# Optimization experiments

Measured on AMD Instinct MI355X. Metric: run time of the kernel, lower is better.

## Reference

```python
import jax, jax.numpy as jnp
from jax import lax
import numpy as np

N_CENTER, N_NEAR, COUT = 1024, 32, 256


def fps(xyz, m):
    # farthest point sampling -> [B, m] int32 indices
    B, N, _ = xyz.shape
    dist0 = jnp.full((B, N), 1e10, xyz.dtype)
    far0 = jnp.zeros((B,), jnp.int32)

    def step(carry, _):
        dists, far = carry
        cen = jax.vmap(lambda p, i: p[i])(xyz, far)            # [B,3]
        d = jnp.sum((xyz - cen[:, None, :]) ** 2, axis=-1)     # [B,N]
        dists = jnp.minimum(dists, d)
        nxt = jnp.argmax(dists, axis=-1).astype(jnp.int32)
        return (dists, nxt), far

    _, idx = lax.scan(step, (dist0, far0), None, length=m)
    return jnp.transpose(idx)                                   # [B,m]


def knn(xyz, k):
    # euclidean kNN over all points -> [B,N,k] (stand-in for surface_knn)
    sq = jnp.sum(xyz ** 2, axis=-1)                             # [B,N]
    d = sq[:, :, None] + sq[:, None, :] - 2.0 * jnp.einsum('bnd,bmd->bnm', xyz, xyz)
    _, idx = lax.top_k(-d, k)
    return idx


def gather(x, idx):
    # index_points: x [B,N,...], idx [B,S] or [B,S,K]
    return jax.vmap(lambda p, i: p[i])(x, idx)


def point_attention(center_fea, group_fea, wq, wk, wv):
    # center_fea [B,S,Cin], group_fea [B,S,K,D] -> [B,S,COUT]
    q = jnp.einsum('bsc,ch->bsh', center_fea, wq)
    k = jnp.einsum('bskd,dh->bskh', group_fea, wk)
    v = jnp.einsum('bskd,dh->bskh', group_fea, wv)
    scores = jnp.einsum('bsh,bskh->bsk', q, k) / jnp.sqrt(jnp.asarray(COUT, q.dtype))
    attn = jax.nn.softmax(scores, axis=-1)
    return jnp.einsum('bsk,bskh->bsh', attn, v)


def _forward(xyz, mad, adj, pt, mad_fea, adj_fea, pt_fea, cst_fea,
             wq_mad, wk_mad, wv_mad, wq_adj, wk_adj, wv_adj,
             wq_pt, wk_pt, wv_pt, wq_cst, wk_cst, wv_cst):
    idx_all = knn(xyz, N_NEAR)                  # [B,N,K]
    fps_idx = fps(xyz, N_CENTER)                # [B,S]

    center_xyz = gather(xyz, fps_idx)
    center_mad = gather(mad, fps_idx)
    center_adj = gather(adj, fps_idx)
    center_pt = gather(pt, fps_idx)
    c_mad_fea = gather(mad_fea, fps_idx)
    c_adj_fea = gather(adj_fea, fps_idx)
    c_pt_fea = gather(pt_fea, fps_idx)
    c_cst_fea = gather(cst_fea, fps_idx)

    idx = gather(idx_all, fps_idx)              # [B,S,K]
    g_xyz = gather(xyz, idx)
    g_mad = gather(mad, idx)
    g_adj = gather(adj, idx)
    g_pt = gather(pt, idx)
    g_mad_fea = gather(mad_fea, idx)
    g_adj_fea = gather(adj_fea, idx)
    g_pt_fea = gather(pt_fea, idx)
    g_cst_fea = gather(cst_fea, idx)

    mad_rel = g_mad - center_mad[:, :, None, :]
    adj_cat = jnp.concatenate([g_adj, jnp.broadcast_to(center_adj[:, :, None, :], g_adj.shape)], axis=-1)
    pt_cat = jnp.concatenate([g_pt, jnp.broadcast_to(center_pt[:, :, None, :], g_pt.shape)], axis=-1)
    xyz_rel = g_xyz - center_xyz[:, :, None, :]

    g_mad_fea = jnp.concatenate([g_mad_fea, mad_rel], axis=-1)
    g_adj_fea = jnp.concatenate([g_adj_fea, adj_cat], axis=-1)
    g_pt_fea = jnp.concatenate([g_pt_fea, pt_cat], axis=-1)
    g_cst_fea = jnp.concatenate([g_cst_fea, xyz_rel], axis=-1)

    o_mad = point_attention(c_mad_fea, g_mad_fea, wq_mad, wk_mad, wv_mad)
    o_adj = point_attention(c_adj_fea, g_adj_fea, wq_adj, wk_adj, wv_adj)
    o_pt = point_attention(c_pt_fea, g_pt_fea, wq_pt, wk_pt, wv_pt)
    o_cst = point_attention(c_cst_fea, g_cst_fea, wq_cst, wk_cst, wv_cst)

    return (center_xyz, center_mad, center_adj, center_pt, o_mad, o_adj, o_pt, o_cst)


def setup_inputs() -> dict:
    key = jax.random.key(0)
    ks = jax.random.split(key, 24)
    B, N, C = 4, 4096, 128
    inp = {
        'xyz': jax.random.normal(ks[0], (B, N, 3), jnp.float32),
        'mad': jax.random.normal(ks[1], (B, N, 3), jnp.float32),
        'adj': jax.random.uniform(ks[2], (B, N, 2), jnp.float32),
        'pt': jax.random.uniform(ks[3], (B, N, 4), jnp.float32),
        'mad_fea': jax.random.normal(ks[4], (B, N, C), jnp.float32),
        'adj_fea': jax.random.normal(ks[5], (B, N, C), jnp.float32),
        'pt_fea': jax.random.normal(ks[6], (B, N, C), jnp.float32),
        'cst_fea': jax.random.normal(ks[7], (B, N, C), jnp.float32),
    }
    dims = {'wq_mad': C, 'wk_mad': C + 3, 'wv_mad': C + 3,
            'wq_adj': C, 'wk_adj': C + 4, 'wv_adj': C + 4,
            'wq_pt': C, 'wk_pt': C + 8, 'wv_pt': C + 8,
            'wq_cst': C, 'wk_cst': C + 3, 'wv_cst': C + 3}
    for i, (name, d) in enumerate(dims.items()):
        inp[name] = jax.random.normal(ks[8 + i], (d, COUT), jnp.float32) * 0.02
    return inp


def reference(xyz, mad, adj, pt, mad_fea, adj_fea, pt_fea, cst_fea,
              wq_mad, wk_mad, wv_mad, wq_adj, wk_adj, wv_adj,
              wq_pt, wk_pt, wv_pt, wq_cst, wk_cst, wv_cst):
    return _forward(xyz, mad, adj, pt, mad_fea, adj_fea, pt_fea, cst_fea,
                    wq_mad, wk_mad, wv_mad, wq_adj, wk_adj, wv_adj,
                    wq_pt, wk_pt, wv_pt, wq_cst, wk_cst, wv_cst)
```

## Files before the change

### kernel.cpp

```cpp
#include <hip/hip_runtime.h>

#define BATCH 4
#define NPTS  4096
#define NC    1024
#define KNN   32
#define CIN   128
#define CO    256

#define OFF_CXYZ 0
#define OFF_CMAD (BATCH*NC*3)
#define OFF_CADJ (OFF_CMAD + BATCH*NC*3)
#define OFF_CPT  (OFF_CADJ + BATCH*NC*2)
#define OFF_OMAD (OFF_CPT  + BATCH*NC*4)
#define OFF_OADJ (OFF_OMAD + BATCH*NC*CO)
#define OFF_OPT  (OFF_OADJ + BATCH*NC*CO)
#define OFF_OCST (OFF_OPT  + BATCH*NC*CO)

typedef unsigned long long u64;

template<bool MAXI>
__device__ __forceinline__ u64 wave_red_u64(u64 k)
{
    const int oldv = MAXI ? 0 : -1;
#define DPP_STEP(C)                                                              \
    {                                                                            \
        unsigned plo = (unsigned)__builtin_amdgcn_update_dpp(oldv, (int)(unsigned)k,        C, 0xf, 0xf, false); \
        unsigned phi = (unsigned)__builtin_amdgcn_update_dpp(oldv, (int)(unsigned)(k>>32),  C, 0xf, 0xf, false); \
        u64 p = ((u64)phi << 32) | plo;                                          \
        if (MAXI ? (p > k) : (p < k)) k = p;                                     \
    }
    DPP_STEP(0x111) DPP_STEP(0x112) DPP_STEP(0x114)
    DPP_STEP(0x118) DPP_STEP(0x142) DPP_STEP(0x143)
#undef DPP_STEP
    return k;
}

__global__ __launch_bounds__(256) void fps_kernel(const float* __restrict__ xyz,
                                                  int* __restrict__ fps_idx)
{
    const int b = blockIdx.x;
    const int t = threadIdx.x;
    const float* xb = xyz + (size_t)b * NPTS * 3;

    __shared__ float4 s_xyz[NPTS];
    __shared__ u64    s_ck[2][4];

    float px[16], py[16], pz[16], dd[16];
    unsigned inv[16];
#pragma unroll
    for (int i = 0; i < 16; ++i) {
        int p = t + i * 256;
        px[i] = xb[p*3+0]; py[i] = xb[p*3+1]; pz[i] = xb[p*3+2];
        s_xyz[p] = make_float4(px[i], py[i], pz[i], 0.f);
        dd[i] = 1e10f;
        inv[i] = ~(unsigned)p;
    }
    __syncthreads();

    int far = 0;
    float cx = xb[0], cy = xb[1], cz = xb[2];
    for (int s = 0; s < NC; ++s) {
        if (t == 0) fps_idx[b*NC + s] = far;
        u64 K[16];
#pragma unroll
        for (int i = 0; i < 16; ++i) {
            float dx = __fsub_rn(px[i], cx);
            float dy = __fsub_rn(py[i], cy);
            float dz = __fsub_rn(pz[i], cz);
            float d  = __fadd_rn(__fadd_rn(__fmul_rn(dx,dx), __fmul_rn(dy,dy)), __fmul_rn(dz,dz));
            float nd = fminf(dd[i], d);
            dd[i] = nd;
            K[i] = ((u64)__float_as_uint(nd) << 32) | inv[i];
        }
#pragma unroll
        for (int st = 8; st >= 1; st >>= 1)
#pragma unroll
            for (int j = 0; j < st; ++j)
                if (K[j+st] > K[j]) K[j] = K[j+st];
        u64 k = wave_red_u64<true>(K[0]);

        const int buf = s & 1;
        if ((t & 63) == 63) s_ck[buf][t>>6] = k;
        __syncthreads();
        u64 k0 = s_ck[buf][0], k1 = s_ck[buf][1], k2 = s_ck[buf][2], k3 = s_ck[buf][3];
        if (k1 > k0) k0 = k1;
        if (k3 > k2) k2 = k3;
        if (k2 > k0) k0 = k2;
        far = (int)~((unsigned)k0);
        float4 c = s_xyz[far];
        cx = c.x; cy = c.y; cz = c.z;
    }
}

__global__ __launch_bounds__(256) void knn_kernel(const float* __restrict__ xyz,
                                                  const int* __restrict__ fps_idx,
                                                  int* __restrict__ nbr_idx)
{
    const int bs = blockIdx.x;
    const int b  = bs >> 10;
    const int t  = threadIdx.x;
    const float* xb = xyz + (size_t)b * NPTS * 3;
    const int ci = fps_idx[bs];
    const float cx = xb[ci*3], cy = xb[ci*3+1], cz = xb[ci*3+2];
    const float sqc = __fadd_rn(__fadd_rn(__fmul_rn(cx,cx), __fmul_rn(cy,cy)), __fmul_rn(cz,cz));

    u64 key[16];
#pragma unroll
    for (int i = 0; i < 16; ++i) {
        int p = t + i * 256;
        float x = xb[p*3], y = xb[p*3+1], z = xb[p*3+2];
        float sqm = __fadd_rn(__fadd_rn(__fmul_rn(x,x), __fmul_rn(y,y)), __fmul_rn(z,z));
        float dot = __fadd_rn(__fadd_rn(__fmul_rn(cx,x), __fmul_rn(cy,y)), __fmul_rn(cz,z));
        float dv  = __fsub_rn(__fadd_rn(sqc, sqm), __fmul_rn(2.0f, dot));
        unsigned u = __float_as_uint(dv);
        u ^= (unsigned)(((int)u >> 31)) | 0x80000000u;
        key[i] = ((u64)u << 32) | (unsigned)p;
    }

    __shared__ u64 s_ck[2][4];

    for (int kk = 0; kk < KNN; ++kk) {
        u64 K[16];
#pragma unroll
        for (int i = 0; i < 16; ++i) K[i] = key[i];
#pragma unroll
        for (int st = 8; st >= 1; st >>= 1)
#pragma unroll
            for (int j = 0; j < st; ++j)
                if (K[j+st] < K[j]) K[j] = K[j+st];
        u64 k = wave_red_u64<false>(K[0]);

        const int buf = kk & 1;
        if ((t & 63) == 63) s_ck[buf][t>>6] = k;
        __syncthreads();
        u64 k0 = s_ck[buf][0], k1 = s_ck[buf][1], k2 = s_ck[buf][2], k3 = s_ck[buf][3];
        if (k1 < k0) k0 = k1;
        if (k3 < k2) k2 = k3;
        if (k2 < k0) k0 = k2;
        unsigned w = (unsigned)k0;
        if (t == 0) nbr_idx[bs*KNN + kk] = (int)w;
#pragma unroll
        for (int i = 0; i < 16; ++i)
            if (w == (unsigned)(t + i*256)) key[i] = ~0ull;
    }
}

template<int TYPE>
__device__ __forceinline__ void attn_type4(
    int b, int bs0,
    const float* __restrict__ fea, const float* __restrict__ aux,
    const float* __restrict__ Wq, const float* __restrict__ Wk, const float* __restrict__ Wv,
    float* __restrict__ outp,
    float (*s_cf)[CIN], float (*s_q)[CO], float (*s_u)[136], float (*s_fea)[KNN][136],
    float (*s_sc)[KNN], float (*s_caux)[4], float (*s_wf)[136],
    const int (*s_nbr)[KNN], const int* s_ci4)
{
    constexpr int D    = (TYPE==2) ? 136 : (TYPE==1) ? 132 : 131;
    constexpr int AUXC = (TYPE==2) ? 4   : (TYPE==1) ? 2   : 3;
    const int t = threadIdx.x;
    const int g32 = t >> 5, l = t & 31;

    {
        int i0 = t, i1 = t + 256;
        s_cf[i0>>7][i0&127] = fea[(size_t)(b*NPTS + s_ci4[i0>>7])*CIN + (i0&127)];
        s_cf[i1>>7][i1&127] = fea[(size_t)(b*NPTS + s_ci4[i1>>7])*CIN + (i1&127)];
    }
    if (t < 16 && (t&3) < AUXC)
        s_caux[t>>2][t&3] = aux[(size_t)(b*NPTS + s_ci4[t>>2])*AUXC + (t&3)];
    __syncthreads();

    float q0=0.f, q1=0.f, q2=0.f, q3=0.f;
#pragma unroll 8
    for (int c = 0; c < CIN; ++c) {
        float w = Wq[c*CO + t];
        q0 = fmaf(s_cf[0][c], w, q0); q1 = fmaf(s_cf[1][c], w, q1);
        q2 = fmaf(s_cf[2][c], w, q2); q3 = fmaf(s_cf[3][c], w, q3);
    }
    s_q[0][t]=q0; s_q[1][t]=q1; s_q[2][t]=q2; s_q[3][t]=q3;
    __syncthreads();

    for (int d0 = 0; d0 < D; d0 += 8) {
        int d = d0 + g32;
        float a0=0.f, a1=0.f, a2=0.f, a3=0.f;
        if (d < D) {
            const float* wr = Wk + (size_t)d * CO;
#pragma unroll
            for (int h = l; h < CO; h += 32) {
                float w = wr[h];
                a0 = fmaf(w, s_q[0][h], a0); a1 = fmaf(w, s_q[1][h], a1);
                a2 = fmaf(w, s_q[2][h], a2); a3 = fmaf(w, s_q[3][h], a3);
            }
        }
#pragma unroll
        for (int off = 16; off; off >>= 1) {
            a0 += __shfl_xor(a0, off); a1 += __shfl_xor(a1, off);
            a2 += __shfl_xor(a2, off); a3 += __shfl_xor(a3, off);
        }
        if (l == 0 && d < D) { s_u[0][d]=a0; s_u[1][d]=a1; s_u[2][d]=a2; s_u[3][d]=a3; }
    }

#pragma unroll
    for (int j = 0; j < 16; ++j) {
        int i4 = t + j*256;
        int g = i4 >> 10, kk = (i4 >> 5) & 31, c4 = i4 & 31;
        const float4 v = *(const float4*)&fea[(size_t)(b*NPTS + s_nbr[g][kk])*CIN + c4*4];
        *(float4*)&s_fea[g][kk][c4*4] = v;
    }
    if (t < 128) {
        int g = t >> 5, kk = t & 31, j = s_nbr[g][kk];
        if (TYPE == 0 || TYPE == 3) {
#pragma unroll
            for (int i2 = 0; i2 < 3; ++i2)
                s_fea[g][kk][CIN+i2] = aux[(size_t)(b*NPTS + j)*3 + i2] - s_caux[g][i2];
        } else if (TYPE == 1) {
            s_fea[g][kk][CIN+0] = aux[(size_t)(b*NPTS + j)*2 + 0];
            s_fea[g][kk][CIN+1] = aux[(size_t)(b*NPTS + j)*2 + 1];
            s_fea[g][kk][CIN+2] = s_caux[g][0];
            s_fea[g][kk][CIN+3] = s_caux[g][1];
        } else {
#pragma unroll
            for (int i2 = 0; i2 < 4; ++i2) s_fea[g][kk][CIN+i2]   = aux[(size_t)(b*NPTS + j)*4 + i2];
#pragma unroll
            for (int i2 = 0; i2 < 4; ++i2) s_fea[g][kk][CIN+4+i2] = s_caux[g][i2];
        }
    }
    __syncthreads();

#pragma unroll
    for (int it = 0; it < 16; ++it) {
        int idx = it*8 + g32;
        int g = idx >> 5, kk = idx & 31;
        float acc = 0.f;
        for (int d = l; d < D; d += 32) acc = fmaf(s_fea[g][kk][d], s_u[g][d], acc);
#pragma unroll
        for (int off = 16; off; off >>= 1) acc += __shfl_xor(acc, off);
        if (l == 0) s_sc[g][kk] = acc * 0.0625f;
    }
    __syncthreads();

    if (t < 128) {
        int g = t >> 5, kk = t & 31;
        float sc = s_sc[g][kk];
        float m = sc;
#pragma unroll
        for (int off = 16; off; off >>= 1) m = fmaxf(m, __shfl_xor(m, off));
        float e = expf(sc - m);
        float ssum = e;
#pragma unroll
        for (int off = 16; off; off >>= 1) ssum += __shfl_xor(ssum, off);
        s_sc[g][kk] = e / ssum;
    }
    __syncthreads();

    {
        int g = t >> 6, l64 = t & 63;
        for (int d = l64; d < D; d += 64) {
            float wf = 0.f;
#pragma unroll
            for (int kk = 0; kk < KNN; ++kk) wf = fmaf(s_sc[g][kk], s_fea[g][kk][d], wf);
            s_wf[g][d] = wf;
        }
    }
    __syncthreads();

    float o0=0.f, o1=0.f, o2=0.f, o3=0.f;
#pragma unroll 8
    for (int d = 0; d < D; ++d) {
        float w = Wv[(size_t)d*CO + t];
        o0 = fmaf(s_wf[0][d], w, o0); o1 = fmaf(s_wf[1][d], w, o1);
        o2 = fmaf(s_wf[2][d], w, o2); o3 = fmaf(s_wf[3][d], w, o3);
    }
    outp[(size_t)(bs0+0)*CO + t] = o0;
    outp[(size_t)(bs0+1)*CO + t] = o1;
    outp[(size_t)(bs0+2)*CO + t] = o2;
    outp[(size_t)(bs0+3)*CO + t] = o3;
    __syncthreads();
}

__global__ __launch_bounds__(256) void attn_kernel(
    const float* __restrict__ xyz, const float* __restrict__ mad,
    const float* __restrict__ adj, const float* __restrict__ pt,
    const float* __restrict__ mad_fea, const float* __restrict__ adj_fea,
    const float* __restrict__ pt_fea,  const float* __restrict__ cst_fea,
    const float* __restrict__ wq_mad, const float* __restrict__ wk_mad, const float* __restrict__ wv_mad,
    const float* __restrict__ wq_adj, const float* __restrict__ wk_adj, const float* __restrict__ wv_adj,
    const float* __restrict__ wq_pt,  const float* __restrict__ wk_pt,  const float* __restrict__ wv_pt,
    const float* __restrict__ wq_cst, const float* __restrict__ wk_cst, const float* __restrict__ wv_cst,
    const int* __restrict__ fps_idx, const int* __restrict__ nbr_idx,
    float* __restrict__ out)
{
    __shared__ float s_cf[4][CIN];
    __shared__ float s_q[4][CO];
    __shared__ float s_u[4][136];
    __shared__ float s_fea[4][KNN][136];
    __shared__ float s_sc[4][KNN];
    __shared__ float s_caux[4][4];
    __shared__ float s_wf[4][136];
    __shared__ int   s_nbr[4][KNN];
    __shared__ int   s_ci4[4];

    const int bs0 = blockIdx.x * 4;
    const int b   = bs0 >> 10;
    const int t   = threadIdx.x;

    if (t < 4) s_ci4[t] = fps_idx[bs0 + t];
    if (t < 128) s_nbr[t>>5][t&31] = nbr_idx[(bs0 + (t>>5))*KNN + (t&31)];
    __syncthreads();

    {
        int g = t >> 6, l64 = t & 63;
        int ci = s_ci4[g], bsg = bs0 + g;
        if (l64 < 3)              out[OFF_CXYZ + bsg*3 + l64]       = xyz[(size_t)(b*NPTS+ci)*3 + l64];
        if (l64 >= 4 && l64 < 7)  out[OFF_CMAD + bsg*3 + (l64-4)]   = mad[(size_t)(b*NPTS+ci)*3 + (l64-4)];
        if (l64 >= 8 && l64 < 10) out[OFF_CADJ + bsg*2 + (l64-8)]   = adj[(size_t)(b*NPTS+ci)*2 + (l64-8)];
        if (l64 >= 12 && l64 < 16)out[OFF_CPT  + bsg*4 + (l64-12)]  = pt[(size_t)(b*NPTS+ci)*4 + (l64-12)];
    }

    attn_type4<0>(b, bs0, mad_fea, mad, wq_mad, wk_mad, wv_mad, out + OFF_OMAD,
                  s_cf, s_q, s_u, s_fea, s_sc, s_caux, s_wf, s_nbr, s_ci4);
    attn_type4<1>(b, bs0, adj_fea, adj, wq_adj, wk_adj, wv_adj, out + OFF_OADJ,
                  s_cf, s_q, s_u, s_fea, s_sc, s_caux, s_wf, s_nbr, s_ci4);
    attn_type4<2>(b, bs0, pt_fea,  pt,  wq_pt,  wk_pt,  wv_pt,  out + OFF_OPT,
                  s_cf, s_q, s_u, s_fea, s_sc, s_caux, s_wf, s_nbr, s_ci4);
    attn_type4<3>(b, bs0, cst_fea, xyz, wq_cst, wk_cst, wv_cst, out + OFF_OCST,
                  s_cf, s_q, s_u, s_fea, s_sc, s_caux, s_wf, s_nbr, s_ci4);
}

extern "C" void kernel_launch(void* const* d_in, const int* in_sizes, int n_in,
                              void* d_out, int out_size, void* d_ws, size_t ws_size,
                              hipStream_t stream)
{
    const float* xyz     = (const float*)d_in[0];
    const float* mad     = (const float*)d_in[1];
    const float* adj     = (const float*)d_in[2];
    const float* pt      = (const float*)d_in[3];
    const float* mad_fea = (const float*)d_in[4];
    const float* adj_fea = (const float*)d_in[5];
    const float* pt_fea  = (const float*)d_in[6];
    const float* cst_fea = (const float*)d_in[7];
    const float* wq_mad  = (const float*)d_in[8];
    const float* wk_mad  = (const float*)d_in[9];
    const float* wv_mad  = (const float*)d_in[10];
    const float* wq_adj  = (const float*)d_in[11];
    const float* wk_adj  = (const float*)d_in[12];
    const float* wv_adj  = (const float*)d_in[13];
    const float* wq_pt   = (const float*)d_in[14];
    const float* wk_pt   = (const float*)d_in[15];
    const float* wv_pt   = (const float*)d_in[16];
    const float* wq_cst  = (const float*)d_in[17];
    const float* wk_cst  = (const float*)d_in[18];
    const float* wv_cst  = (const float*)d_in[19];
    float* out = (float*)d_out;

    int* fps_idx = (int*)d_ws;
    int* nbr_idx = fps_idx + BATCH*NC;

    fps_kernel<<<BATCH, 256, 0, stream>>>(xyz, fps_idx);
    knn_kernel<<<BATCH*NC, 256, 0, stream>>>(xyz, fps_idx, nbr_idx);
    attn_kernel<<<BATCH*NC/4, 256, 0, stream>>>(xyz, mad, adj, pt,
        mad_fea, adj_fea, pt_fea, cst_fea,
        wq_mad, wk_mad, wv_mad, wq_adj, wk_adj, wv_adj,
        wq_pt, wk_pt, wv_pt, wq_cst, wk_cst, wv_cst,
        fps_idx, nbr_idx, out);
}
```

Before: 1.153 ms.

## Precompute Wq·Wkᵀ per type, incremental kNN min, restructure attention per wave

Folds the query and key projections into a precomputed matrix M = Wq·Wkᵀ per feature type. These are computed by extra blocks launched alongside the FPS kernel, together with zero-padded copies of Wv. The attention kernel then computes u = cf·M directly instead of a Q projection followed by a K contraction, and gives one wave to each center with float4 shared-memory access. The kNN selection keeps a per-thread running minimum and rescans its 16 keys only in the thread that owned the chosen point, instead of rescanning every round. The cost is extra workspace and work added to the latency-bound FPS launch.

```diff
diff --git a/kernel.cpp b/kernel.cpp
--- a/kernel.cpp
+++ b/kernel.cpp
@@ -6,6 +6,7 @@
 #define KNN   32
 #define CIN   128
 #define CO    256
+#define DP    136
 
 #define OFF_CXYZ 0
 #define OFF_CMAD (BATCH*NC*3)
@@ -35,15 +36,53 @@
     return k;
 }
 
-__global__ __launch_bounds__(256) void fps_kernel(const float* __restrict__ xyz,
-                                                  int* __restrict__ fps_idx)
-{
-    const int b = blockIdx.x;
-    const int t = threadIdx.x;
-    const float* xb = xyz + (size_t)b * NPTS * 3;
-
+__global__ __launch_bounds__(256) void fps_prep_kernel(
+    const float* __restrict__ xyz, int* __restrict__ fps_idx,
+    const float* __restrict__ wq_mad, const float* __restrict__ wk_mad, const float* __restrict__ wv_mad,
+    const float* __restrict__ wq_adj, const float* __restrict__ wk_adj, const float* __restrict__ wv_adj,
+    const float* __restrict__ wq_pt,  const float* __restrict__ wk_pt,  const float* __restrict__ wv_pt,
+    const float* __restrict__ wq_cst, const float* __restrict__ wk_cst, const float* __restrict__ wv_cst,
+    float* __restrict__ M, float* __restrict__ Wvp)
+{
     __shared__ float4 s_xyz[NPTS];
     __shared__ u64    s_ck[2][4];
+    const int t = threadIdx.x;
+
+    if (blockIdx.x >= BATCH) {
+        const int r    = blockIdx.x - BATCH;
+        const int type = r / DP;
+        const int row  = r - type * DP;
+        const float* wq; const float* wk; const float* wv; int D;
+        if (type == 0)      { wq=wq_mad; wk=wk_mad; wv=wv_mad; D=131; }
+        else if (type == 1) { wq=wq_adj; wk=wk_adj; wv=wv_adj; D=132; }
+        else if (type == 2) { wq=wq_pt;  wk=wk_pt;  wv=wv_pt;  D=136; }
+        else                { wq=wq_cst; wk=wk_cst; wv=wv_cst; D=131; }
+
+        Wvp[((size_t)type*DP + row)*CO + t] = (row < D) ? wv[(size_t)row*CO + t] : 0.f;
+
+        if (row < CIN) {
+            float* sq = (float*)s_xyz;
+            sq[t] = wq[(size_t)row*CO + t];
+            __syncthreads();
+            if (t < DP) {
+                float acc = 0.f;
+                if (t < D) {
+                    const float* wkr = wk + (size_t)t * CO;
+                    for (int h = 0; h < CO; h += 4) {
+                        float4 a = *(const float4*)&wkr[h];
+                        float4 b4 = *(const float4*)&sq[h];
+                        acc = fmaf(a.x,b4.x,acc); acc = fmaf(a.y,b4.y,acc);
+                        acc = fmaf(a.z,b4.z,acc); acc = fmaf(a.w,b4.w,acc);
+                    }
+                }
+                M[((size_t)type*CIN + row)*DP + t] = acc;
+            }
+        }
+        return;
+    }
+
+    const int b = blockIdx.x;
+    const float* xb = xyz + (size_t)b * NPTS * 3;
 
     float px[16], py[16], pz[16], dd[16];
     unsigned inv[16];
@@ -116,20 +155,14 @@
         u ^= (unsigned)(((int)u >> 31)) | 0x80000000u;
         key[i] = ((u64)u << 32) | (unsigned)p;
     }
+    u64 kmin = key[0];
+#pragma unroll
+    for (int i = 1; i < 16; ++i) if (key[i] < kmin) kmin = key[i];
 
     __shared__ u64 s_ck[2][4];
 
     for (int kk = 0; kk < KNN; ++kk) {
-        u64 K[16];
-#pragma unroll
-        for (int i = 0; i < 16; ++i) K[i] = key[i];
-#pragma unroll
-        for (int st = 8; st >= 1; st >>= 1)
-#pragma unroll
-            for (int j = 0; j < st; ++j)
-                if (K[j+st] < K[j]) K[j] = K[j+st];
-        u64 k = wave_red_u64<false>(K[0]);
-
+        u64 k = wave_red_u64<false>(kmin);
         const int buf = kk & 1;
         if ((t & 63) == 63) s_ck[buf][t>>6] = k;
         __syncthreads();
@@ -139,108 +172,101 @@
         if (k2 < k0) k0 = k2;
         unsigned w = (unsigned)k0;
         if (t == 0) nbr_idx[bs*KNN + kk] = (int)w;
-#pragma unroll
-        for (int i = 0; i < 16; ++i)
-            if (w == (unsigned)(t + i*256)) key[i] = ~0ull;
+        if ((w & 255u) == (unsigned)t) {
+#pragma unroll
+            for (int i = 0; i < 16; ++i)
+                if (w == (unsigned)(t + i*256)) key[i] = ~0ull;
+            u64 m = key[0];
+#pragma unroll
+            for (int i = 1; i < 16; ++i) if (key[i] < m) m = key[i];
+            kmin = m;
+        }
     }
 }
 
 template<int TYPE>
-__device__ __forceinline__ void attn_type4(
-    int b, int bs0,
+__device__ __forceinline__ void attn_t(
+    int b, int bs0, int ci,
     const float* __restrict__ fea, const float* __restrict__ aux,
-    const float* __restrict__ Wq, const float* __restrict__ Wk, const float* __restrict__ Wv,
+    const float* __restrict__ Mt, const float* __restrict__ Wvpt,
     float* __restrict__ outp,
-    float (*s_cf)[CIN], float (*s_q)[CO], float (*s_u)[136], float (*s_fea)[KNN][136],
-    float (*s_sc)[KNN], float (*s_caux)[4], float (*s_wf)[136],
-    const int (*s_nbr)[KNN], const int* s_ci4)
-{
-    constexpr int D    = (TYPE==2) ? 136 : (TYPE==1) ? 132 : 131;
-    constexpr int AUXC = (TYPE==2) ? 4   : (TYPE==1) ? 2   : 3;
-    const int t = threadIdx.x;
-    const int g32 = t >> 5, l = t & 31;
-
-    {
-        int i0 = t, i1 = t + 256;
-        s_cf[i0>>7][i0&127] = fea[(size_t)(b*NPTS + s_ci4[i0>>7])*CIN + (i0&127)];
-        s_cf[i1>>7][i1&127] = fea[(size_t)(b*NPTS + s_ci4[i1>>7])*CIN + (i1&127)];
-    }
-    if (t < 16 && (t&3) < AUXC)
-        s_caux[t>>2][t&3] = aux[(size_t)(b*NPTS + s_ci4[t>>2])*AUXC + (t&3)];
-    __syncthreads();
-
-    float q0=0.f, q1=0.f, q2=0.f, q3=0.f;
-#pragma unroll 8
-    for (int c = 0; c < CIN; ++c) {
-        float w = Wq[c*CO + t];
-        q0 = fmaf(s_cf[0][c], w, q0); q1 = fmaf(s_cf[1][c], w, q1);
-        q2 = fmaf(s_cf[2][c], w, q2); q3 = fmaf(s_cf[3][c], w, q3);
-    }
-    s_q[0][t]=q0; s_q[1][t]=q1; s_q[2][t]=q2; s_q[3][t]=q3;
-    __syncthreads();
-
-    for (int d0 = 0; d0 < D; d0 += 8) {
-        int d = d0 + g32;
-        float a0=0.f, a1=0.f, a2=0.f, a3=0.f;
-        if (d < D) {
-            const float* wr = Wk + (size_t)d * CO;
-#pragma unroll
-            for (int h = l; h < CO; h += 32) {
-                float w = wr[h];
-                a0 = fmaf(w, s_q[0][h], a0); a1 = fmaf(w, s_q[1][h], a1);
-                a2 = fmaf(w, s_q[2][h], a2); a3 = fmaf(w, s_q[3][h], a3);
+    float (*s_cf)[CIN], float (*s_u)[DP], float (*s_fea)[KNN][DP],
+    float (*s_sc)[KNN], float (*s_wf)[DP], const int (*s_nbr4)[KNN])
+{
+    const int t = threadIdx.x, g = t >> 6, l = t & 63;
+    const int l31 = l & 31, h32 = l >> 5;
+
+    if (l < 32) {
+        float4 v = *(const float4*)&fea[((size_t)(b*NPTS + ci))*CIN + l*4];
+        *(float4*)&s_cf[g][l*4] = v;
+    }
+#pragma unroll
+    for (int it = 0; it < 16; ++it) {
+        int kk = it*2 + h32;
+        int j  = s_nbr4[g][kk];
+        float4 v = *(const float4*)&fea[((size_t)(b*NPTS + j))*CIN + l31*4];
+        *(float4*)&s_fea[g][kk][l31*4] = v;
+    }
+    if (l < KNN) {
+        int j = s_nbr4[g][l];
+        float pad[8];
+        if (TYPE == 0 || TYPE == 3) {
+#pragma unroll
+            for (int i = 0; i < 3; ++i)
+                pad[i] = aux[(size_t)(b*NPTS + j)*3 + i] - aux[(size_t)(b*NPTS + ci)*3 + i];
+            pad[3]=pad[4]=pad[5]=pad[6]=pad[7]=0.f;
+        } else if (TYPE == 1) {
+            pad[0] = aux[(size_t)(b*NPTS + j)*2 + 0];
+            pad[1] = aux[(size_t)(b*NPTS + j)*2 + 1];
+            pad[2] = aux[(size_t)(b*NPTS + ci)*2 + 0];
+            pad[3] = aux[(size_t)(b*NPTS + ci)*2 + 1];
+            pad[4]=pad[5]=pad[6]=pad[7]=0.f;
+        } else {
+#pragma unroll
+            for (int i = 0; i < 4; ++i) pad[i]   = aux[(size_t)(b*NPTS + j)*4 + i];
+#pragma unroll
+            for (int i = 0; i < 4; ++i) pad[4+i] = aux[(size_t)(b*NPTS + ci)*4 + i];
+        }
+#pragma unroll
+        for (int i = 0; i < 8; ++i) s_fea[g][l][CIN+i] = pad[i];
+    }
+    __syncthreads();
+
+#pragma unroll
+    for (int j = 0; j < 3; ++j) {
+        int d = l + 64*j;
+        if (d < DP) {
+            float acc = 0.f;
+            for (int c = 0; c < CIN; c += 4) {
+                float4 cf4 = *(const float4*)&s_cf[g][c];
+                acc = fmaf(cf4.x, Mt[(size_t)(c+0)*DP + d], acc);
+                acc = fmaf(cf4.y, Mt[(size_t)(c+1)*DP + d], acc);
+                acc = fmaf(cf4.z, Mt[(size_t)(c+2)*DP + d], acc);
+                acc = fmaf(cf4.w, Mt[(size_t)(c+3)*DP + d], acc);
             }
-        }
-#pragma unroll
-        for (int off = 16; off; off >>= 1) {
-            a0 += __shfl_xor(a0, off); a1 += __shfl_xor(a1, off);
-            a2 += __shfl_xor(a2, off); a3 += __shfl_xor(a3, off);
-        }
-        if (l == 0 && d < D) { s_u[0][d]=a0; s_u[1][d]=a1; s_u[2][d]=a2; s_u[3][d]=a3; }
-    }
-
-#pragma unroll
-    for (int j = 0; j < 16; ++j) {
-        int i4 = t + j*256;
-        int g = i4 >> 10, kk = (i4 >> 5) & 31, c4 = i4 & 31;
-        const float4 v = *(const float4*)&fea[(size_t)(b*NPTS + s_nbr[g][kk])*CIN + c4*4];
-        *(float4*)&s_fea[g][kk][c4*4] = v;
-    }
-    if (t < 128) {
-        int g = t >> 5, kk = t & 31, j = s_nbr[g][kk];
-        if (TYPE == 0 || TYPE == 3) {
-#pragma unroll
-            for (int i2 = 0; i2 < 3; ++i2)
-                s_fea[g][kk][CIN+i2] = aux[(size_t)(b*NPTS + j)*3 + i2] - s_caux[g][i2];
-        } else if (TYPE == 1) {
-            s_fea[g][kk][CIN+0] = aux[(size_t)(b*NPTS + j)*2 + 0];
-            s_fea[g][kk][CIN+1] = aux[(size_t)(b*NPTS + j)*2 + 1];
-            s_fea[g][kk][CIN+2] = s_caux[g][0];
-            s_fea[g][kk][CIN+3] = s_caux[g][1];
-        } else {
-#pragma unroll
-            for (int i2 = 0; i2 < 4; ++i2) s_fea[g][kk][CIN+i2]   = aux[(size_t)(b*NPTS + j)*4 + i2];
-#pragma unroll
-            for (int i2 = 0; i2 < 4; ++i2) s_fea[g][kk][CIN+4+i2] = s_caux[g][i2];
+            s_u[g][d] = acc;
         }
     }
     __syncthreads();
 
 #pragma unroll
     for (int it = 0; it < 16; ++it) {
-        int idx = it*8 + g32;
-        int g = idx >> 5, kk = idx & 31;
+        int kk = it*2 + h32;
         float acc = 0.f;
-        for (int d = l; d < D; d += 32) acc = fmaf(s_fea[g][kk][d], s_u[g][d], acc);
+        for (int c = l31; c < DP/4; c += 32) {
+            float4 f4 = *(const float4*)&s_fea[g][kk][c*4];
+            float4 u4 = *(const float4*)&s_u[g][c*4];
+            acc = fmaf(f4.x,u4.x,acc); acc = fmaf(f4.y,u4.y,acc);
+            acc = fmaf(f4.z,u4.z,acc); acc = fmaf(f4.w,u4.w,acc);
+        }
 #pragma unroll
         for (int off = 16; off; off >>= 1) acc += __shfl_xor(acc, off);
-        if (l == 0) s_sc[g][kk] = acc * 0.0625f;
-    }
-    __syncthreads();
-
-    if (t < 128) {
-        int g = t >> 5, kk = t & 31;
-        float sc = s_sc[g][kk];
+        if (l31 == 0) s_sc[g][kk] = acc * 0.0625f;
+    }
+    __syncthreads();
+
+    if (l < KNN) {
+        float sc = s_sc[g][l];
         float m = sc;
 #pragma unroll
         for (int off = 16; off; off >>= 1) m = fmaxf(m, __shfl_xor(m, off));
@@ -248,27 +274,43 @@
         float ssum = e;
 #pragma unroll
         for (int off = 16; off; off >>= 1) ssum += __shfl_xor(ssum, off);
-        s_sc[g][kk] = e / ssum;
-    }
-    __syncthreads();
-
-    {
-        int g = t >> 6, l64 = t & 63;
-        for (int d = l64; d < D; d += 64) {
-            float wf = 0.f;
-#pragma unroll
-            for (int kk = 0; kk < KNN; ++kk) wf = fmaf(s_sc[g][kk], s_fea[g][kk][d], wf);
-            s_wf[g][d] = wf;
-        }
+        s_sc[g][l] = e / ssum;
+    }
+    __syncthreads();
+
+    if (l < DP/4) {
+        const int d0 = l*4;
+        float w0=0.f, w1=0.f, w2=0.f, w3=0.f;
+#pragma unroll
+        for (int k4 = 0; k4 < KNN; k4 += 4) {
+            float4 a  = *(const float4*)&s_sc[g][k4];
+            float4 f0 = *(const float4*)&s_fea[g][k4+0][d0];
+            float4 f1 = *(const float4*)&s_fea[g][k4+1][d0];
+            float4 f2 = *(const float4*)&s_fea[g][k4+2][d0];
+            float4 f3 = *(const float4*)&s_fea[g][k4+3][d0];
+            w0=fmaf(a.x,f0.x,w0); w1=fmaf(a.x,f0.y,w1); w2=fmaf(a.x,f0.z,w2); w3=fmaf(a.x,f0.w,w3);
+            w0=fmaf(a.y,f1.x,w0); w1=fmaf(a.y,f1.y,w1); w2=fmaf(a.y,f1.z,w2); w3=fmaf(a.y,f1.w,w3);
+            w0=fmaf(a.z,f2.x,w0); w1=fmaf(a.z,f2.y,w1); w2=fmaf(a.z,f2.z,w2); w3=fmaf(a.z,f2.w,w3);
+            w0=fmaf(a.w,f3.x,w0); w1=fmaf(a.w,f3.y,w1); w2=fmaf(a.w,f3.z,w2); w3=fmaf(a.w,f3.w,w3);
+        }
+        s_wf[g][d0+0]=w0; s_wf[g][d0+1]=w1; s_wf[g][d0+2]=w2; s_wf[g][d0+3]=w3;
     }
     __syncthreads();
 
     float o0=0.f, o1=0.f, o2=0.f, o3=0.f;
-#pragma unroll 8
-    for (int d = 0; d < D; ++d) {
-        float w = Wv[(size_t)d*CO + t];
-        o0 = fmaf(s_wf[0][d], w, o0); o1 = fmaf(s_wf[1][d], w, o1);
-        o2 = fmaf(s_wf[2][d], w, o2); o3 = fmaf(s_wf[3][d], w, o3);
+    for (int d4 = 0; d4 < DP/4; ++d4) {
+        float4 wf0 = *(const float4*)&s_wf[0][d4*4];
+        float4 wf1 = *(const float4*)&s_wf[1][d4*4];
+        float4 wf2 = *(const float4*)&s_wf[2][d4*4];
+        float4 wf3 = *(const float4*)&s_wf[3][d4*4];
+        float v0 = Wvpt[(size_t)(d4*4+0)*CO + t];
+        float v1 = Wvpt[(size_t)(d4*4+1)*CO + t];
+        float v2 = Wvpt[(size_t)(d4*4+2)*CO + t];
+        float v3 = Wvpt[(size_t)(d4*4+3)*CO + t];
+        o0=fmaf(wf0.x,v0,o0); o0=fmaf(wf0.y,v1,o0); o0=fmaf(wf0.z,v2,o0); o0=fmaf(wf0.w,v3,o0);
+        o1=fmaf(wf1.x,v0,o1); o1=fmaf(wf1.y,v1,o1); o1=fmaf(wf1.z,v2,o1); o1=fmaf(wf1.w,v3,o1);
+        o2=fmaf(wf2.x,v0,o2); o2=fmaf(wf2.y,v1,o2); o2=fmaf(wf2.z,v2,o2); o2=fmaf(wf2.w,v3,o2);
+        o3=fmaf(wf3.x,v0,o3); o3=fmaf(wf3.y,v1,o3); o3=fmaf(wf3.z,v2,o3); o3=fmaf(wf3.w,v3,o3);
     }
     outp[(size_t)(bs0+0)*CO + t] = o0;
     outp[(size_t)(bs0+1)*CO + t] = o1;
@@ -282,48 +324,41 @@
     const float* __restrict__ adj, const float* __restrict__ pt,
     const float* __restrict__ mad_fea, const float* __restrict__ adj_fea,
     const float* __restrict__ pt_fea,  const float* __restrict__ cst_fea,
-    const float* __restrict__ wq_mad, const float* __restrict__ wk_mad, const float* __restrict__ wv_mad,
-    const float* __restrict__ wq_adj, const float* __restrict__ wk_adj, const float* __restrict__ wv_adj,
-    const float* __restrict__ wq_pt,  const float* __restrict__ wk_pt,  const float* __restrict__ wv_pt,
-    const float* __restrict__ wq_cst, const float* __restrict__ wk_cst, const float* __restrict__ wv_cst,
+    const float* __restrict__ M, const float* __restrict__ Wvp,
     const int* __restrict__ fps_idx, const int* __restrict__ nbr_idx,
     float* __restrict__ out)
 {
     __shared__ float s_cf[4][CIN];
-    __shared__ float s_q[4][CO];
-    __shared__ float s_u[4][136];
-    __shared__ float s_fea[4][KNN][136];
+    __shared__ float s_u[4][DP];
+    __shared__ float s_fea[4][KNN][DP];
     __shared__ float s_sc[4][KNN];
-    __shared__ float s_caux[4][4];
-    __shared__ float s_wf[4][136];
-    __shared__ int   s_nbr[4][KNN];
+    __shared__ float s_wf[4][DP];
+    __shared__ int   s_nbr4[4][KNN];
     __shared__ int   s_ci4[4];
 
     const int bs0 = blockIdx.x * 4;
     const int b   = bs0 >> 10;
     const int t   = threadIdx.x;
+    const int g   = t >> 6, l = t & 63;
 
     if (t < 4) s_ci4[t] = fps_idx[bs0 + t];
-    if (t < 128) s_nbr[t>>5][t&31] = nbr_idx[(bs0 + (t>>5))*KNN + (t&31)];
-    __syncthreads();
-
-    {
-        int g = t >> 6, l64 = t & 63;
-        int ci = s_ci4[g], bsg = bs0 + g;
-        if (l64 < 3)              out[OFF_CXYZ + bsg*3 + l64]       = xyz[(size_t)(b*NPTS+ci)*3 + l64];
-        if (l64 >= 4 && l64 < 7)  out[OFF_CMAD + bsg*3 + (l64-4)]   = mad[(size_t)(b*NPTS+ci)*3 + (l64-4)];
-        if (l64 >= 8 && l64 < 10) out[OFF_CADJ + bsg*2 + (l64-8)]   = adj[(size_t)(b*NPTS+ci)*2 + (l64-8)];
-        if (l64 >= 12 && l64 < 16)out[OFF_CPT  + bsg*4 + (l64-12)]  = pt[(size_t)(b*NPTS+ci)*4 + (l64-12)];
-    }
-
-    attn_type4<0>(b, bs0, mad_fea, mad, wq_mad, wk_mad, wv_mad, out + OFF_OMAD,
-                  s_cf, s_q, s_u, s_fea, s_sc, s_caux, s_wf, s_nbr, s_ci4);
-    attn_type4<1>(b, bs0, adj_fea, adj, wq_adj, wk_adj, wv_adj, out + OFF_OADJ,
-                  s_cf, s_q, s_u, s_fea, s_sc, s_caux, s_wf, s_nbr, s_ci4);
-    attn_type4<2>(b, bs0, pt_fea,  pt,  wq_pt,  wk_pt,  wv_pt,  out + OFF_OPT,
-                  s_cf, s_q, s_u, s_fea, s_sc, s_caux, s_wf, s_nbr, s_ci4);
-    attn_type4<3>(b, bs0, cst_fea, xyz, wq_cst, wk_cst, wv_cst, out + OFF_OCST,
-                  s_cf, s_q, s_u, s_fea, s_sc, s_caux, s_wf, s_nbr, s_ci4);
+    if (t < 128) s_nbr4[t>>5][t&31] = nbr_idx[(bs0 + (t>>5))*KNN + (t&31)];
+    __syncthreads();
+    const int ci = s_ci4[g];
+
+    if (l < 3)             out[OFF_CXYZ + (bs0+g)*3 + l]      = xyz[(size_t)(b*NPTS+ci)*3 + l];
+    if (l >= 4 && l < 7)   out[OFF_CMAD + (bs0+g)*3 + (l-4)]  = mad[(size_t)(b*NPTS+ci)*3 + (l-4)];
+    if (l >= 8 && l < 10)  out[OFF_CADJ + (bs0+g)*2 + (l-8)]  = adj[(size_t)(b*NPTS+ci)*2 + (l-8)];
+    if (l >= 12 && l < 16) out[OFF_CPT  + (bs0+g)*4 + (l-12)] = pt[(size_t)(b*NPTS+ci)*4 + (l-12)];
+
+    attn_t<0>(b, bs0, ci, mad_fea, mad, M + 0*CIN*DP, Wvp + 0*DP*CO, out + OFF_OMAD,
+              s_cf, s_u, s_fea, s_sc, s_wf, s_nbr4);
+    attn_t<1>(b, bs0, ci, adj_fea, adj, M + 1*CIN*DP, Wvp + 1*DP*CO, out + OFF_OADJ,
+              s_cf, s_u, s_fea, s_sc, s_wf, s_nbr4);
+    attn_t<2>(b, bs0, ci, pt_fea,  pt,  M + 2*CIN*DP, Wvp + 2*DP*CO, out + OFF_OPT,
+              s_cf, s_u, s_fea, s_sc, s_wf, s_nbr4);
+    attn_t<3>(b, bs0, ci, cst_fea, xyz, M + 3*CIN*DP, Wvp + 3*DP*CO, out + OFF_OCST,
+              s_cf, s_u, s_fea, s_sc, s_wf, s_nbr4);
 }
 
 extern "C" void kernel_launch(void* const* d_in, const int* in_sizes, int n_in,
@@ -352,14 +387,15 @@
     const float* wv_cst  = (const float*)d_in[19];
     float* out = (float*)d_out;
 
-    int* fps_idx = (int*)d_ws;
-    int* nbr_idx = fps_idx + BATCH*NC;
-
-    fps_kernel<<<BATCH, 256, 0, stream>>>(xyz, fps_idx);
+    int*   fps_idx = (int*)d_ws;
+    int*   nbr_idx = fps_idx + BATCH*NC;
+    float* M       = (float*)(nbr_idx + BATCH*NC*KNN);
+    float* Wvp     = M + 4*CIN*DP;
+
+    fps_prep_kernel<<<BATCH + 4*DP, 256, 0, stream>>>(xyz, fps_idx,
+        wq_mad, wk_mad, wv_mad, wq_adj, wk_adj, wv_adj,
+        wq_pt, wk_pt, wv_pt, wq_cst, wk_cst, wv_cst, M, Wvp);
     knn_kernel<<<BATCH*NC, 256, 0, stream>>>(xyz, fps_idx, nbr_idx);
     attn_kernel<<<BATCH*NC/4, 256, 0, stream>>>(xyz, mad, adj, pt,
-        mad_fea, adj_fea, pt_fea, cst_fea,
-        wq_mad, wk_mad, wv_mad, wq_adj, wk_adj, wv_adj,
-        wq_pt, wk_pt, wv_pt, wq_cst, wk_cst, wv_cst,
-        fps_idx, nbr_idx, out);
-}
+        mad_fea, adj_fea, pt_fea, cst_fea, M, Wvp, fps_idx, nbr_idx, out);
+}
```

Result: faster. 1.120 ms (-2.9%).
